# Optimization experiments

Hardware: AMD Instinct MI355X
Metric: run time of the kernel (lower is better)

Reference implementation:

```python
import jax, jax.numpy as jnp
import numpy as np


def setup_inputs() -> dict:
    key = jax.random.key(0)
    k1, k2 = jax.random.split(key)
    pc1 = jax.random.normal(k1, (8, 2048, 3), dtype=jnp.float32)
    pc2 = jax.random.normal(k2, (8, 2048, 3), dtype=jnp.float32)
    return {"pc1": pc1, "pc2": pc2}


def reference(pc1, pc2):
    # Flatten to point lists, matching pc.reshape(-1, 3)
    p1 = pc1.reshape(-1, 3)  # [N1, 3]
    p2 = pc2.reshape(-1, 3)  # [N2, 3]
    # Squared pairwise distances via ||a||^2 + ||b||^2 - 2 a.b
    sq1 = jnp.sum(p1 * p1, axis=-1)  # [N1]
    sq2 = jnp.sum(p2 * p2, axis=-1)  # [N2]
    d2 = sq1[:, None] + sq2[None, :] - 2.0 * jnp.einsum('nd,md->nm', p1, p2)  # [N1, N2]
    d2 = jnp.maximum(d2, 0.0)
    d = jnp.sqrt(d2)  # Euclidean, matching cKDTree.query distances
    # dist1 = NN distance from each pc2 point into pc1 (tree1.query(pc2))
    dist1 = jnp.min(d, axis=0)  # [N2]
    # dist2 = NN distance from each pc1 point into pc2 (tree2.query(pc1))
    dist2 = jnp.min(d, axis=1)  # [N1]
    return jnp.mean(dist1) + jnp.mean(dist2)
```

## Files before the change

### kernel.cpp

```cpp
#include <hip/hip_runtime.h>
#include <math.h>

#define N_PTS 16384
#define TPB   256
#define IP    8
#define ROWS_B (TPB * IP)
#define IBLK  (N_PTS / ROWS_B)
#define JT    128
#define JS    (N_PTS / JT)
#define NCH   (JT / 2)
#define REDB  64

typedef float f32x2 __attribute__((ext_vector_type(2)));
typedef float f32x4 __attribute__((ext_vector_type(4)));

#define PK_ADD2(dst, a, b)                                                 \
  asm("v_pk_add_f32 %0, %1, %2" : "=v"(dst) : "v"(a), "v"(b))
#define PK_FMA2A(acc, a, b)                                                \
  asm("v_pk_fma_f32 %0, %1, %2, %0" : "+v"(acc) : "v"(a), "v"(b))
#define MIN3A(acc, a, b)                                                   \
  asm("v_min3_f32 %0, %1, %2, %0" : "+v"(acc) : "v"(a), "v"(b))

__global__ __launch_bounds__(TPB, 4) void chamfer_min(
    const float* __restrict__ p1, const float* __restrict__ p2,
    unsigned int* __restrict__ dmin, float* __restrict__ outp) {
  __shared__ f32x4 pkA[NCH];
  __shared__ f32x4 pkB[NCH];
  __shared__ unsigned int cmin[JT];

  if (blockIdx.x == 0 && blockIdx.y == 0 && threadIdx.x == 0)
    outp[0] = 0.f;

  const int jbase = blockIdx.x * JT;
  if (threadIdx.x < NCH) {
    int t = threadIdx.x;
    int ja = jbase + t, jb = jbase + t + NCH;
    float xa = p2[3 * ja], ya = p2[3 * ja + 1], za = p2[3 * ja + 2];
    float xb = p2[3 * jb], yb = p2[3 * jb + 1], zb = p2[3 * jb + 2];
    pkA[t] = (f32x4){xa, xb, ya, yb};
    pkB[t] = (f32x4){za, zb, 0.5f * (xa * xa + ya * ya + za * za),
                             0.5f * (xb * xb + yb * yb + zb * zb)};
  }
  if (threadIdx.x < JT) cmin[threadIdx.x] = 0x7F800000u;

  const int ibase = blockIdx.y * ROWS_B;
  f32x2 nx2[IP], ny2[IP], nz2[IP], h2[IP];
  float rmin[IP];
#pragma unroll
  for (int m = 0; m < IP; ++m) {
    int r = ibase + m * TPB + threadIdx.x;
    float x = p1[3 * r + 0], y = p1[3 * r + 1], z = p1[3 * r + 2];
    nx2[m] = (f32x2){-x, -x};
    ny2[m] = (f32x2){-y, -y};
    nz2[m] = (f32x2){-z, -z};
    float h = 0.5f * (x * x + y * y + z * z);
    h2[m] = (f32x2){h, h};
    rmin[m] = INFINITY;
  }
  __syncthreads();

  const int lane = threadIdx.x & 63;
  const int base = lane + ((threadIdx.x >> 6) << 4);
  const int nxtb = ((lane + 1) & 63) << 2;

  float Aa = INFINITY, Ab = INFINITY;
  const int p0 = base & (NCH - 1);
  f32x4 qA = pkA[p0], qB = pkB[p0];
#pragma unroll 2
  for (int s = 0; s < NCH; ++s) {
    float cpa = __int_as_float(__builtin_amdgcn_ds_bpermute(nxtb, __float_as_int(Aa)));
    float cpb = __int_as_float(__builtin_amdgcn_ds_bpermute(nxtb, __float_as_int(Ab)));
    f32x2 X = qA.xy, Y = qA.zw, Z = qB.xy, W = qB.zw;
    const int pn = (base + s + 1) & (NCH - 1);
    qA = pkA[pn];
    qB = pkB[pn];
#pragma unroll
    for (int m = 0; m < IP; m += 2) {
      f32x2 s0, s1;
      PK_ADD2(s0, h2[m], W);
      PK_FMA2A(s0, nx2[m], X);
      PK_FMA2A(s0, ny2[m], Y);
      PK_FMA2A(s0, nz2[m], Z);
      PK_ADD2(s1, h2[m + 1], W);
      PK_FMA2A(s1, nx2[m + 1], X);
      PK_FMA2A(s1, ny2[m + 1], Y);
      PK_FMA2A(s1, nz2[m + 1], Z);
      MIN3A(rmin[m],     s0.x, s0.y);
      MIN3A(rmin[m + 1], s1.x, s1.y);
      MIN3A(cpa, s0.x, s1.x);
      MIN3A(cpb, s0.y, s1.y);
    }
    Aa = cpa; Ab = cpb;
  }

  {
    const int pe = (base + NCH - 1) & (NCH - 1);
    atomicMin(&cmin[pe],       __float_as_uint(fmaxf(Aa, 0.f)));
    atomicMin(&cmin[pe + NCH], __float_as_uint(fmaxf(Ab, 0.f)));
  }

#pragma unroll
  for (int m = 0; m < IP; ++m) {
    float d2 = fmaxf(0.f, 2.f * rmin[m]);
    atomicMin(&dmin[ibase + m * TPB + threadIdx.x], __float_as_uint(d2));
  }

  __syncthreads();
  for (int t = threadIdx.x; t < JT; t += TPB) {
    float v = __uint_as_float(cmin[t]);
    atomicMin(&dmin[N_PTS + jbase + t], __float_as_uint(2.f * v));
  }
}

__global__ __launch_bounds__(TPB) void chamfer_reduce(
    const unsigned int* __restrict__ dmin, float* __restrict__ outp) {
  float s = 0.f;
  for (int i = blockIdx.x * TPB + threadIdx.x; i < 2 * N_PTS; i += REDB * TPB)
    s += sqrtf(__uint_as_float(dmin[i]));
#pragma unroll
  for (int off = 32; off > 0; off >>= 1)
    s += __shfl_down(s, off, 64);
  __shared__ float partial[TPB / 64];
  if ((threadIdx.x & 63) == 0) partial[threadIdx.x >> 6] = s;
  __syncthreads();
  if (threadIdx.x == 0) {
    float t = 0.f;
    for (int w = 0; w < TPB / 64; ++w) t += partial[w];
    atomicAdd(outp, t * (1.0f / (float)N_PTS));
  }
}

extern "C" void kernel_launch(void* const* d_in, const int* in_sizes, int n_in,
                              void* d_out, int out_size, void* d_ws, size_t ws_size,
                              hipStream_t stream) {
  const float* pc1 = (const float*)d_in[0];
  const float* pc2 = (const float*)d_in[1];
  unsigned int* dmin = (unsigned int*)d_ws;

  chamfer_min<<<dim3(JS, IBLK), TPB, 0, stream>>>(pc1, pc2, dmin, (float*)d_out);
  chamfer_reduce<<<REDB, TPB, 0, stream>>>(dmin, (float*)d_out);
}
```

Measured before the change: 87.37 us.

## Replace bpermute rotation with XOR Gray-code traversal using DPP and swizzle

The column-min accumulator used to rotate around the wave each step with two ds_bpermute ops. Now the lanes walk the 64 column pairs in an XOR (Gray-code) order. Exchanges with XOR 1 and 2 use DPP quad permutes, XOR 4 uses ds_swizzle, and larger XORs use shfl_xor. The aim is to take the LDS-routed permute latency and traffic off the inner loop, while the LDS reads switch to XOR addressing. The loop is fully unrolled into 8 substeps, which raises code size.

```diff
diff --git a/kernel.cpp b/kernel.cpp
--- a/kernel.cpp
+++ b/kernel.cpp
@@ -20,6 +20,12 @@
   asm("v_pk_fma_f32 %0, %1, %2, %0" : "+v"(acc) : "v"(a), "v"(b))
 #define MIN3A(acc, a, b)                                                   \
   asm("v_min3_f32 %0, %1, %2, %0" : "+v"(acc) : "v"(a), "v"(b))
+
+#define XDPP(v, CTRL)                                                      \
+  v = __int_as_float(__builtin_amdgcn_update_dpp(                          \
+      0, __float_as_int(v), CTRL, 0xF, 0xF, true))
+#define XSWZ(v)                                                            \
+  v = __int_as_float(__builtin_amdgcn_ds_swizzle(__float_as_int(v), 0x101F))
 
 __global__ __launch_bounds__(TPB, 4) void chamfer_min(
     const float* __restrict__ p1, const float* __restrict__ p2,
@@ -60,44 +66,57 @@
   __syncthreads();
 
   const int lane = threadIdx.x & 63;
-  const int base = lane + ((threadIdx.x >> 6) << 4);
-  const int nxtb = ((lane + 1) & 63) << 2;
+  const int base = lane ^ ((threadIdx.x >> 6) << 4);
+  int pos = base;
+  float Aa = INFINITY, Ab = INFINITY;
+  f32x4 qA, qB;
 
-  float Aa = INFINITY, Ab = INFINITY;
-  const int p0 = base & (NCH - 1);
-  f32x4 qA = pkA[p0], qB = pkB[p0];
-#pragma unroll 2
-  for (int s = 0; s < NCH; ++s) {
-    float cpa = __int_as_float(__builtin_amdgcn_ds_bpermute(nxtb, __float_as_int(Aa)));
-    float cpb = __int_as_float(__builtin_amdgcn_ds_bpermute(nxtb, __float_as_int(Ab)));
-    f32x2 X = qA.xy, Y = qA.zw, Z = qB.xy, W = qB.zw;
-    const int pn = (base + s + 1) & (NCH - 1);
-    qA = pkA[pn];
-    qB = pkB[pn];
-#pragma unroll
-    for (int m = 0; m < IP; m += 2) {
-      f32x2 s0, s1;
-      PK_ADD2(s0, h2[m], W);
-      PK_FMA2A(s0, nx2[m], X);
-      PK_FMA2A(s0, ny2[m], Y);
-      PK_FMA2A(s0, nz2[m], Z);
-      PK_ADD2(s1, h2[m + 1], W);
-      PK_FMA2A(s1, nx2[m + 1], X);
-      PK_FMA2A(s1, ny2[m + 1], Y);
-      PK_FMA2A(s1, nz2[m + 1], Z);
-      MIN3A(rmin[m],     s0.x, s0.y);
-      MIN3A(rmin[m + 1], s1.x, s1.y);
-      MIN3A(cpa, s0.x, s1.x);
-      MIN3A(cpb, s0.y, s1.y);
-    }
-    Aa = cpa; Ab = cpb;
+#define BODY()                                                             \
+  {                                                                        \
+    f32x2 X = qA.xy, Y = qA.zw, Z = qB.xy, W = qB.zw;                      \
+    _Pragma("unroll")                                                      \
+    for (int m = 0; m < IP; m += 2) {                                      \
+      f32x2 s0, s1;                                                        \
+      PK_ADD2(s0, h2[m], W);                                               \
+      PK_FMA2A(s0, nx2[m], X);                                             \
+      PK_FMA2A(s0, ny2[m], Y);                                             \
+      PK_FMA2A(s0, nz2[m], Z);                                             \
+      PK_ADD2(s1, h2[m + 1], W);                                           \
+      PK_FMA2A(s1, nx2[m + 1], X);                                         \
+      PK_FMA2A(s1, ny2[m + 1], Y);                                         \
+      PK_FMA2A(s1, nz2[m + 1], Z);                                         \
+      MIN3A(rmin[m],     s0.x, s0.y);                                      \
+      MIN3A(rmin[m + 1], s1.x, s1.y);                                      \
+      MIN3A(Aa, s0.x, s1.x);                                               \
+      MIN3A(Ab, s0.y, s1.y);                                               \
+    }                                                                      \
+  }
+#define SUBSTEP(D)                                                         \
+  {                                                                        \
+    if ((D) == 1)      { XDPP(Aa, 0xB1); XDPP(Ab, 0xB1); }                 \
+    else if ((D) == 2) { XDPP(Aa, 0x4E); XDPP(Ab, 0x4E); }                 \
+    else               { XSWZ(Aa);       XSWZ(Ab); }                       \
+    pos ^= (D);                                                            \
+    qA = pkA[pos]; qB = pkB[pos];                                          \
+    BODY();                                                                \
   }
 
-  {
-    const int pe = (base + NCH - 1) & (NCH - 1);
-    atomicMin(&cmin[pe],       __float_as_uint(fmaxf(Aa, 0.f)));
-    atomicMin(&cmin[pe + NCH], __float_as_uint(fmaxf(Ab, 0.f)));
+#pragma unroll 1
+  for (int t = 0; t < 8; ++t) {
+    if (t) {
+      const int dh = 8 << __builtin_ctz(t);
+      Aa = __shfl_xor(Aa, dh, 64);
+      Ab = __shfl_xor(Ab, dh, 64);
+      pos ^= dh;
+    }
+    qA = pkA[pos]; qB = pkB[pos];
+    BODY();
+    SUBSTEP(1); SUBSTEP(2); SUBSTEP(1); SUBSTEP(4);
+    SUBSTEP(1); SUBSTEP(2); SUBSTEP(1);
   }
+
+  atomicMin(&cmin[pos],       __float_as_uint(fmaxf(Aa, 0.f)));
+  atomicMin(&cmin[pos + NCH], __float_as_uint(fmaxf(Ab, 0.f)));
 
 #pragma unroll
   for (int m = 0; m < IP; ++m) {
```

Result: no change. 87.35 us (-0.0%).
